# Performance work log

Measured on AMD Instinct MI355X. Metric: run time of the kernel, lower is better.

The kernel has to match this reference:

```python
import jax, jax.numpy as jnp
import numpy as np

NUM_FEAT = 10
C_IN = 64


def setup_inputs() -> dict:
    key = jax.random.key(0)
    ks = jax.random.split(key, 8)
    B, T, C, H, W = 1, 8, C_IN, 32, 32
    scale = 1.0 / np.sqrt(C)
    return {
        "input1": jax.random.normal(ks[0], (B, T, C, H, W), dtype=jnp.float32),
        "input2": jax.random.normal(ks[1], (B, T, C, H, W), dtype=jnp.float32),
        "w1": jax.random.normal(ks[2], (NUM_FEAT, C), dtype=jnp.float32) * scale,
        "b1": jax.random.normal(ks[3], (NUM_FEAT,), dtype=jnp.float32) * scale,
        "w2": jax.random.normal(ks[4], (NUM_FEAT, C), dtype=jnp.float32) * scale,
        "b2": jax.random.normal(ks[5], (NUM_FEAT,), dtype=jnp.float32) * scale,
        "w3": jax.random.normal(ks[6], (NUM_FEAT, C), dtype=jnp.float32) * scale,
        "b3": jax.random.normal(ks[7], (NUM_FEAT,), dtype=jnp.float32) * scale,
    }


def reference(input1, input2, w1, b1, w2, b2, w3, b3):
    B, T, C, H, W = input1.shape
    N = T * H * W
    # transpose(1,2).reshape -> [B, C, T*H*W]
    x1 = input1.transpose(0, 2, 1, 3, 4).reshape(B, C, N)
    x2 = input2.transpose(0, 2, 1, 3, 4).reshape(B, C, N)
    # 1x1 Conv1d projections (act == 0 -> ReLU branch)
    q = jnp.einsum('fc,bcn->bnf', w1, x1) + b1            # [B, N, F]
    k = jnp.einsum('fc,bcn->bfn', w2, x2) + b2[:, None]   # [B, F, N]
    v = jnp.einsum('fc,bcn->bnf', w3, x1) + b3            # [B, N, F]
    scores = jax.nn.relu(jnp.einsum('bnf,bfm->bnm', q, k))  # [B, N, N]
    out = jnp.einsum('bnm,bmf->bnf', scores, v)             # [B, N, F]
    # view([B,T,H,W,F]).permute(0,1,4,2,3)
    return out.reshape(B, T, H, W, -1).transpose(0, 1, 4, 2, 3)
```

## Files before the change

### kernel.cpp

```cpp
#include <hip/hip_runtime.h>

typedef float v2f __attribute__((ext_vector_type(2)));
typedef float v4f __attribute__((ext_vector_type(4)));

#define NF     10
#define NF2    5
#define NPAD   16
#define CIN    64
#define N_TOT  8192
#define HW     1024
#define MTILE  128
#define MSPLIT 16
#define MCHUNK (N_TOT / MSPLIT)

__global__ __launch_bounds__(256) void qkv_kernel(
    const float* __restrict__ in1, const float* __restrict__ in2,
    const float* __restrict__ w1, const float* __restrict__ b1,
    const float* __restrict__ w2, const float* __restrict__ b2,
    const float* __restrict__ w3, const float* __restrict__ b3,
    float* __restrict__ qd, float* __restrict__ kd, float* __restrict__ vd)
{
    const int which = blockIdx.y;
    const float* x = (which == 1) ? in2 : in1;
    const float* w = (which == 0) ? w1 : ((which == 1) ? w2 : w3);
    const float* b = (which == 0) ? b1 : ((which == 1) ? b2 : b3);
    float* dst     = (which == 0) ? qd : ((which == 1) ? kd : vd);

    const int n  = blockIdx.x * 256 + threadIdx.x;
    const int t  = n >> 10;
    const int hw = n & 1023;
    const float* p = x + (size_t)t * (CIN * HW) + hw;

    float acc[NF];
#pragma unroll
    for (int f = 0; f < NF; ++f) acc[f] = b[f];

#pragma unroll 8
    for (int c = 0; c < CIN; ++c) {
        float a = p[c * HW];
#pragma unroll
        for (int f = 0; f < NF; ++f)
            acc[f] = fmaf(w[f * CIN + c], a, acc[f]);
    }

    float* o = dst + (size_t)n * NPAD;
#pragma unroll
    for (int f = 0; f < NF; ++f) o[f] = acc[f];
#pragma unroll
    for (int f = NF; f < NPAD; ++f) o[f] = 0.f;
}

__global__ __launch_bounds__(256) void attn_kernel(
    const float* __restrict__ qd, const float* __restrict__ kd,
    const float* __restrict__ vd, float* __restrict__ out)
{
    __shared__ v2f ks[MTILE][NPAD / 2];
    __shared__ v2f vs[MTILE][NPAD / 2];

    const int tid = threadIdx.x;
    const int n   = blockIdx.x * 256 + tid;
    const int m0  = blockIdx.y * MCHUNK;

    v2f q2[NF2];
#pragma unroll
    for (int j = 0; j < NF2; ++j)
        q2[j] = *(const v2f*)(qd + (size_t)n * NPAD + 2 * j);

    v2f acc[NF2];
#pragma unroll
    for (int j = 0; j < NF2; ++j) acc[j] = (v2f)(0.f);

    for (int mt = 0; mt < MCHUNK; mt += MTILE) {
        const float* kb = kd + (size_t)(m0 + mt) * NPAD;
        const float* vb = vd + (size_t)(m0 + mt) * NPAD;
#pragma unroll
        for (int i = 0; i < 2; ++i) {
            int idx = tid + i * 256;
            ((v4f*)ks)[idx] = ((const v4f*)kb)[idx];
            ((v4f*)vs)[idx] = ((const v4f*)vb)[idx];
        }
        __syncthreads();

#pragma unroll 2
        for (int m = 0; m < MTILE; ++m) {
            v2f d = q2[0] * ks[m][0];
            d = __builtin_elementwise_fma(q2[1], ks[m][1], d);
            d = __builtin_elementwise_fma(q2[2], ks[m][2], d);
            d = __builtin_elementwise_fma(q2[3], ks[m][3], d);
            d = __builtin_elementwise_fma(q2[4], ks[m][4], d);
            float s = fmaxf(d.x + d.y, 0.f);
            v2f s2 = (v2f)(s);
#pragma unroll
            for (int j = 0; j < NF2; ++j)
                acc[j] = __builtin_elementwise_fma(s2, vs[m][j], acc[j]);
        }
        __syncthreads();
    }

    const int t  = n >> 10;
    const int hw = n & 1023;
    float* op = out + (size_t)t * (NF * HW) + hw;
#pragma unroll
    for (int j = 0; j < NF2; ++j) {
        atomicAdd(op + (2 * j) * HW,     acc[j].x);
        atomicAdd(op + (2 * j + 1) * HW, acc[j].y);
    }
}

extern "C" void kernel_launch(void* const* d_in, const int* in_sizes, int n_in,
                              void* d_out, int out_size, void* d_ws, size_t ws_size,
                              hipStream_t stream)
{
    const float* in1 = (const float*)d_in[0];
    const float* in2 = (const float*)d_in[1];
    const float* w1  = (const float*)d_in[2];
    const float* b1  = (const float*)d_in[3];
    const float* w2  = (const float*)d_in[4];
    const float* b2  = (const float*)d_in[5];
    const float* w3  = (const float*)d_in[6];
    const float* b3  = (const float*)d_in[7];

    float* q = (float*)d_ws;
    float* k = q + (size_t)N_TOT * NPAD;
    float* v = k + (size_t)N_TOT * NPAD;
    float* out = (float*)d_out;

    hipMemsetAsync(d_out, 0, (size_t)out_size * sizeof(float), stream);

    qkv_kernel<<<dim3(N_TOT / 256, 3), 256, 0, stream>>>(
        in1, in2, w1, b1, w2, b2, w3, b3, q, k, v);

    attn_kernel<<<dim3(N_TOT / 256, MSPLIT), 256, 0, stream>>>(q, k, v, out);
}
```

Baseline: 126.3 us.

## Compute attention with bf16 MFMA tiles instead of scalar fp32 FMAs

```diff
diff --git a/kernel.cpp b/kernel.cpp
--- a/kernel.cpp
+++ b/kernel.cpp
@@ -1,30 +1,51 @@
 #include <hip/hip_runtime.h>
 
-typedef float v2f __attribute__((ext_vector_type(2)));
-typedef float v4f __attribute__((ext_vector_type(4)));
+typedef short  s4  __attribute__((ext_vector_type(4)));
+typedef float  f4  __attribute__((ext_vector_type(4)));
+typedef unsigned int u2v __attribute__((ext_vector_type(2)));
+typedef unsigned int uint32;
+typedef unsigned short ushort16;
 
 #define NF     10
-#define NF2    5
-#define NPAD   16
 #define CIN    64
-#define N_TOT  8192
+#define NTOT   8192
 #define HW     1024
-#define MTILE  128
-#define MSPLIT 16
-#define MCHUNK (N_TOT / MSPLIT)
+#define FPAD   16
+#define MSPLIT 8
+#define MCHUNK (NTOT / MSPLIT)
 
-__global__ __launch_bounds__(256) void qkv_kernel(
+#if defined(__has_builtin) && __has_builtin(__builtin_amdgcn_mfma_f32_16x16x16bf16_1k)
+#define MFMA16(a, b, c) __builtin_amdgcn_mfma_f32_16x16x16bf16_1k((a), (b), (c), 0, 0, 0)
+#else
+static __device__ inline f4 mfma16_asm(s4 a, s4 b, f4 c) {
+    f4 d;
+    asm volatile("s_nop 1\n\t"
+                 "v_mfma_f32_16x16x16_bf16 %0, %1, %2, %3\n\t"
+                 "s_nop 7\n\ts_nop 7"
+                 : "=v"(d) : "v"(a), "v"(b), "v"(c));
+    return d;
+}
+#define MFMA16(a, b, c) mfma16_asm((a), (b), (c))
+#endif
+
+static __device__ inline ushort16 f32_to_bf16_rne(float x) {
+    uint32 u = __builtin_bit_cast(uint32, x);
+    u = (u + 0x7fffu + ((u >> 16) & 1u)) >> 16;
+    return (ushort16)u;
+}
+
+__global__ __launch_bounds__(256) void qkv_bf16_kernel(
     const float* __restrict__ in1, const float* __restrict__ in2,
     const float* __restrict__ w1, const float* __restrict__ b1,
     const float* __restrict__ w2, const float* __restrict__ b2,
     const float* __restrict__ w3, const float* __restrict__ b3,
-    float* __restrict__ qd, float* __restrict__ kd, float* __restrict__ vd)
+    ushort16* __restrict__ qb, ushort16* __restrict__ kb,
+    ushort16* __restrict__ vT)
 {
     const int which = blockIdx.y;
     const float* x = (which == 1) ? in2 : in1;
     const float* w = (which == 0) ? w1 : ((which == 1) ? w2 : w3);
     const float* b = (which == 0) ? b1 : ((which == 1) ? b2 : b3);
-    float* dst     = (which == 0) ? qd : ((which == 1) ? kd : vd);
 
     const int n  = blockIdx.x * 256 + threadIdx.x;
     const int t  = n >> 10;
@@ -34,76 +55,74 @@
     float acc[NF];
 #pragma unroll
     for (int f = 0; f < NF; ++f) acc[f] = b[f];
-
 #pragma unroll 8
     for (int c = 0; c < CIN; ++c) {
         float a = p[c * HW];
 #pragma unroll
-        for (int f = 0; f < NF; ++f)
-            acc[f] = fmaf(w[f * CIN + c], a, acc[f]);
+        for (int f = 0; f < NF; ++f) acc[f] = fmaf(w[f * CIN + c], a, acc[f]);
     }
 
-    float* o = dst + (size_t)n * NPAD;
+    if (which == 2) {
 #pragma unroll
-    for (int f = 0; f < NF; ++f) o[f] = acc[f];
+        for (int f = 0; f < NF; ++f) vT[(size_t)f * NTOT + n] = f32_to_bf16_rne(acc[f]);
+    } else {
+        ushort16 row[FPAD];
 #pragma unroll
-    for (int f = NF; f < NPAD; ++f) o[f] = 0.f;
+        for (int f = 0; f < NF; ++f) row[f] = f32_to_bf16_rne(acc[f]);
+#pragma unroll
+        for (int f = NF; f < FPAD; ++f) row[f] = 0;
+        ushort16* dst = ((which == 0) ? qb : kb) + (size_t)n * FPAD;
+        ((uint4*)dst)[0] = ((const uint4*)row)[0];
+        ((uint4*)dst)[1] = ((const uint4*)row)[1];
+    }
 }
 
-__global__ __launch_bounds__(256) void attn_kernel(
-    const float* __restrict__ qd, const float* __restrict__ kd,
-    const float* __restrict__ vd, float* __restrict__ out)
+__global__ __launch_bounds__(256) void attn_mfma_kernel(
+    const ushort16* __restrict__ qb, const ushort16* __restrict__ kb,
+    const ushort16* __restrict__ vT, float* __restrict__ out)
 {
-    __shared__ v2f ks[MTILE][NPAD / 2];
-    __shared__ v2f vs[MTILE][NPAD / 2];
+    const int lane = threadIdx.x & 63;
+    const int wid  = threadIdx.x >> 6;
+    const int row  = lane & 15;
+    const int quad = lane >> 4;
+    const int n0   = blockIdx.x * 64 + wid * 16;
+    const int m0   = blockIdx.y * MCHUNK;
 
-    const int tid = threadIdx.x;
-    const int n   = blockIdx.x * 256 + tid;
-    const int m0  = blockIdx.y * MCHUNK;
+    const s4 qf = *(const s4*)(qb + (size_t)(n0 + row) * FPAD + 4 * quad);
 
-    v2f q2[NF2];
-#pragma unroll
-    for (int j = 0; j < NF2; ++j)
-        q2[j] = *(const v2f*)(qd + (size_t)n * NPAD + 2 * j);
+    const s4* kp = (const s4*)(kb + (size_t)(m0 + row) * FPAD + 4 * quad);
+    const s4* vp = (const s4*)(vT + (size_t)row * NTOT + m0 + 4 * quad);
 
-    v2f acc[NF2];
-#pragma unroll
-    for (int j = 0; j < NF2; ++j) acc[j] = (v2f)(0.f);
+    f4 acc  = {0.f, 0.f, 0.f, 0.f};
+    const f4 zero = {0.f, 0.f, 0.f, 0.f};
 
-    for (int mt = 0; mt < MCHUNK; mt += MTILE) {
-        const float* kb = kd + (size_t)(m0 + mt) * NPAD;
-        const float* vb = vd + (size_t)(m0 + mt) * NPAD;
-#pragma unroll
-        for (int i = 0; i < 2; ++i) {
-            int idx = tid + i * 256;
-            ((v4f*)ks)[idx] = ((const v4f*)kb)[idx];
-            ((v4f*)vs)[idx] = ((const v4f*)vb)[idx];
-        }
-        __syncthreads();
+#pragma unroll 8
+    for (int s = 0; s < MCHUNK / 16; ++s) {
+        s4 kf = kp[s * 64];
+        s4 vf = vp[s * 4];
 
-#pragma unroll 2
-        for (int m = 0; m < MTILE; ++m) {
-            v2f d = q2[0] * ks[m][0];
-            d = __builtin_elementwise_fma(q2[1], ks[m][1], d);
-            d = __builtin_elementwise_fma(q2[2], ks[m][2], d);
-            d = __builtin_elementwise_fma(q2[3], ks[m][3], d);
-            d = __builtin_elementwise_fma(q2[4], ks[m][4], d);
-            float s = fmaxf(d.x + d.y, 0.f);
-            v2f s2 = (v2f)(s);
-#pragma unroll
-            for (int j = 0; j < NF2; ++j)
-                acc[j] = __builtin_elementwise_fma(s2, vs[m][j], acc[j]);
-        }
-        __syncthreads();
+        f4 sc = MFMA16(kf, qf, zero);
+
+        float r0 = fmaxf(sc[0], 0.f), r1 = fmaxf(sc[1], 0.f);
+        float r2 = fmaxf(sc[2], 0.f), r3 = fmaxf(sc[3], 0.f);
+        uint32 lo = __builtin_amdgcn_perm(__builtin_bit_cast(uint32, r1),
+                                          __builtin_bit_cast(uint32, r0), 0x07060302u);
+        uint32 hi = __builtin_amdgcn_perm(__builtin_bit_cast(uint32, r3),
+                                          __builtin_bit_cast(uint32, r2), 0x07060302u);
+        s4 pb = __builtin_bit_cast(s4, (u2v){lo, hi});
+
+        acc = MFMA16(vf, pb, acc);
     }
 
+    const int n  = n0 + row;
     const int t  = n >> 10;
     const int hw = n & 1023;
     float* op = out + (size_t)t * (NF * HW) + hw;
+    const int fbase = 4 * quad;
 #pragma unroll
-    for (int j = 0; j < NF2; ++j) {
-        atomicAdd(op + (2 * j) * HW,     acc[j].x);
-        atomicAdd(op + (2 * j + 1) * HW, acc[j].y);
+    for (int r = 0; r < 4; ++r) {
+        int f = fbase + r;
+        if (f < NF) atomicAdd(op + f * HW, acc[r]);
     }
 }
 
@@ -120,15 +139,15 @@
     const float* w3  = (const float*)d_in[6];
     const float* b3  = (const float*)d_in[7];
 
-    float* q = (float*)d_ws;
-    float* k = q + (size_t)N_TOT * NPAD;
-    float* v = k + (size_t)N_TOT * NPAD;
+    ushort16* qb = (ushort16*)d_ws;
+    ushort16* kb = qb + (size_t)NTOT * FPAD;
+    ushort16* vT = kb + (size_t)NTOT * FPAD;
     float* out = (float*)d_out;
 
     hipMemsetAsync(d_out, 0, (size_t)out_size * sizeof(float), stream);
 
-    qkv_kernel<<<dim3(N_TOT / 256, 3), 256, 0, stream>>>(
-        in1, in2, w1, b1, w2, b2, w3, b3, q, k, v);
+    qkv_bf16_kernel<<<dim3(NTOT / 256, 3), 256, 0, stream>>>(
+        in1, in2, w1, b1, w2, b2, w3, b3, qb, kb, vT);
 
-    attn_kernel<<<dim3(N_TOT / 256, MSPLIT), 256, 0, stream>>>(q, k, v, out);
+    attn_mfma_kernel<<<dim3(NTOT / 64, MSPLIT), 256, 0, stream>>>(qb, kb, vT, out);
 }
```

Result: faster. 115.0 us (-8.9%).
